# Performance work log

Hardware: AMD Instinct MI355X
Metric: run time of the kernel (lower is better)

The kernel has to match this reference:

```python
import jax, jax.numpy as jnp
import numpy as np

N_NODES = 50000
N_EDGES = 800000
D_IN = 128
N_HEADS = 8
D_OUT = 16  # per head; H*D = 128


def setup_inputs() -> dict:
    key = jax.random.key(0)
    ks = jax.random.split(key, 10)
    HD = N_HEADS * D_OUT
    nfeat = jax.random.normal(ks[0], (N_NODES, D_IN), dtype=jnp.float32)
    efeat = jax.random.normal(ks[1], (N_EDGES, D_IN), dtype=jnp.float32)
    src = jax.random.randint(ks[2], (N_EDGES,), 0, N_NODES, dtype=jnp.int32)
    dst = jax.random.randint(ks[3], (N_EDGES,), 0, N_NODES, dtype=jnp.int32)
    # parameters (Xavier-ish scale)
    W_fc = jax.random.normal(ks[4], (D_IN, HD), dtype=jnp.float32) * 0.05
    attn_l = jax.random.normal(ks[5], (N_HEADS, D_OUT), dtype=jnp.float32) * 0.05
    attn_r = jax.random.normal(ks[6], (N_HEADS, D_OUT), dtype=jnp.float32) * 0.05
    bias = jnp.zeros((HD,), dtype=jnp.float32)
    W_e = jax.random.normal(ks[7], (D_IN, HD), dtype=jnp.float32) * 0.05
    b_e = jnp.zeros((HD,), dtype=jnp.float32)
    return {"nfeat": nfeat, "efeat": efeat, "src": src, "dst": dst,
            "W_fc": W_fc, "attn_l": attn_l, "attn_r": attn_r, "bias": bias,
            "W_e": W_e, "b_e": b_e}


def reference(nfeat, efeat, src, dst, W_fc, attn_l, attn_r, bias, W_e, b_e):
    N = nfeat.shape[0]
    E = src.shape[0]
    H, D = attn_l.shape
    # ---- GATConv (DGL semantics, feat_drop=attn_drop=0, no residual/activation) ----
    hf = nfeat @ W_fc                      # [N, H*D]
    h = hf.reshape(N, H, D)                # [N, H, D]
    el = jnp.einsum('nhd,hd->nh', h, attn_l)   # [N, H]
    er = jnp.einsum('nhd,hd->nh', h, attn_r)   # [N, H]
    # per-edge scores: message src -> dst, softmax over incoming edges of dst
    e = jax.nn.leaky_relu(el[src] + er[dst], negative_slope=0.2)  # [E, H]
    m = jax.ops.segment_max(e, dst, num_segments=N)               # [N, H]
    m = jnp.where(jnp.isfinite(m), m, jnp.zeros_like(m))          # empty segments -> 0
    ex = jnp.exp(e - m[dst])                                      # [E, H]
    denom = jax.ops.segment_sum(ex, dst, num_segments=N)          # [N, H]
    a = ex / denom[dst]                                           # [E, H]
    agg = jax.ops.segment_sum(a[:, :, None] * h[src], dst, num_segments=N)  # [N, H, D]
    gat = agg.reshape(N, H * D) + bias                            # flatten(1) + bias
    # ---- skip term: fc(nfeat) / (in_degree + 1) ----
    ones = jnp.ones((E,), dtype=nfeat.dtype)
    indeg = jax.ops.segment_sum(ones, dst, num_segments=N)        # [N]
    sfeat = hf / (indeg + 1.0)[:, None]
    out = gat + sfeat
    # ---- econv: edge feature mean aggregation (copy_e + mean over in-edges) ----
    ef = efeat @ W_e + b_e                                        # [E, H*D]
    esum = jax.ops.segment_sum(ef, dst, num_segments=N)           # [N, H*D]
    h_e = esum / jnp.maximum(indeg, 1.0)[:, None]                 # zero-deg -> 0
    return out + h_e
```

## Files before the change

### kernel.cpp

```cpp
#include <hip/hip_runtime.h>
#include <math.h>

#define NN 50000
#define NE 800000
#define HD 128
#define NH 8
#define DO 16
#define NEG_BIG -3.0e38f

__device__ inline void fma4(float4& a, float s, const float4& b) {
    a.x = fmaf(s, b.x, a.x); a.y = fmaf(s, b.y, a.y);
    a.z = fmaf(s, b.z, a.z); a.w = fmaf(s, b.w, a.w);
}
__device__ inline void red4(float4& a, int off) {
    a.x += __shfl_xor(a.x, off); a.y += __shfl_xor(a.y, off);
    a.z += __shfl_xor(a.z, off); a.w += __shfl_xor(a.w, off);
}

__global__ void init_kernel(int* __restrict__ indeg) {
    int i = blockIdx.x * blockDim.x + threadIdx.x;
    if (i < NN) indeg[i] = 0;
}

__global__ void count_deg_kernel(const int* __restrict__ dst, int* __restrict__ indeg) {
    int e = blockIdx.x * blockDim.x + threadIdx.x;
    if (e < NE) atomicAdd(&indeg[dst[e]], 1);
}

__global__ __launch_bounds__(1024) void scan_kernel(const int* __restrict__ indeg,
                                                    int* __restrict__ offsets,
                                                    int* __restrict__ cursor) {
    __shared__ int part[1024];
    const int t = threadIdx.x;
    const int CH = (NN + 1023) / 1024;
    int b = t * CH, e = min(b + CH, NN);
    int s = 0;
    for (int i = b; i < e; ++i) s += indeg[i];
    part[t] = s;
    __syncthreads();
    for (int off = 1; off < 1024; off <<= 1) {
        int v = (t >= off) ? part[t - off] : 0;
        __syncthreads();
        part[t] += v;
        __syncthreads();
    }
    int base = (t == 0) ? 0 : part[t - 1];
    for (int i = b; i < e; ++i) {
        offsets[i] = base;
        cursor[i] = base;
        base += indeg[i];
    }
    if (t == 1023) offsets[NN] = base;
}

__global__ void scatter_kernel(const int* __restrict__ src, const int* __restrict__ dst,
                               int* __restrict__ cursor, int2* __restrict__ sorted) {
    int e = blockIdx.x * blockDim.x + threadIdx.x;
    if (e < NE) {
        int d = dst[e];
        int pos = atomicAdd(&cursor[d], 1);
        sorted[pos] = make_int2(src[e], e);
    }
}

template<bool FUSE_ATTN, bool ADD>
__global__ __launch_bounds__(256, 3) void gemm64_kernel(
    const float* __restrict__ A, const float* __restrict__ W,
    float* __restrict__ out,
    const float* __restrict__ attn_l, const float* __restrict__ attn_r,
    float* __restrict__ el, float* __restrict__ er)
{
    __shared__ float sA[64 * HD];
    __shared__ float sW[32 * HD];
    const int tid = threadIdx.x;
    const int tc = tid & 15;
    const int tr = tid >> 4;
    const int row0 = blockIdx.x * 64;

    const float4* Av = (const float4*)A;
    float4* sAv = (float4*)sA;
#pragma unroll
    for (int j = 0; j < 8; ++j) {
        int f = tid + j * 256;
        int r = f >> 5, g = f & 31;
        int gr = row0 + r;
        float4 v = make_float4(0.f, 0.f, 0.f, 0.f);
        if (gr < NN) v = Av[(size_t)gr * 32 + g];
        sAv[r * 32 + (g ^ ((r & 3) << 1))] = v;
    }

    float4 acc[4][2];
#pragma unroll
    for (int rj = 0; rj < 4; ++rj) {
        acc[rj][0] = make_float4(0.f, 0.f, 0.f, 0.f);
        acc[rj][1] = make_float4(0.f, 0.f, 0.f, 0.f);
    }

    const float4* Wv = (const float4*)W;
    float4* sWv = (float4*)sW;
    for (int kc = 0; kc < 4; ++kc) {
        __syncthreads();
#pragma unroll
        for (int j = 0; j < 4; ++j) {
            int f = tid + j * 256;
            sWv[f] = Wv[(size_t)(kc * 32 + (f >> 5)) * 32 + (f & 31)];
        }
        __syncthreads();
#pragma unroll 8
        for (int kk = 0; kk < 32; ++kk) {
            float4 w0 = sWv[kk * 32 + tc];
            float4 w1 = sWv[kk * 32 + 16 + tc];
            int k = kc * 32 + kk;
#pragma unroll
            for (int rj = 0; rj < 4; ++rj) {
                int r = tr + rj * 16;
                float a = sA[r * HD + (k ^ ((r & 3) << 3))];
                fma4(acc[rj][0], a, w0);
                fma4(acc[rj][1], a, w1);
            }
        }
    }

    if (FUSE_ATTN) {
        const int h1 = tc >> 2, q = tc & 3;
        float4 al0 = ((const float4*)attn_l)[h1 * 4 + q];
        float4 ar0 = ((const float4*)attn_r)[h1 * 4 + q];
        float4 al1 = ((const float4*)attn_l)[(h1 + 4) * 4 + q];
        float4 ar1 = ((const float4*)attn_r)[(h1 + 4) * 4 + q];
#pragma unroll
        for (int rj = 0; rj < 4; ++rj) {
            float sl0 = acc[rj][0].x * al0.x + acc[rj][0].y * al0.y + acc[rj][0].z * al0.z + acc[rj][0].w * al0.w;
            float sr0 = acc[rj][0].x * ar0.x + acc[rj][0].y * ar0.y + acc[rj][0].z * ar0.z + acc[rj][0].w * ar0.w;
            float sl1 = acc[rj][1].x * al1.x + acc[rj][1].y * al1.y + acc[rj][1].z * al1.z + acc[rj][1].w * al1.w;
            float sr1 = acc[rj][1].x * ar1.x + acc[rj][1].y * ar1.y + acc[rj][1].z * ar1.z + acc[rj][1].w * ar1.w;
            sl0 += __shfl_xor(sl0, 1); sl0 += __shfl_xor(sl0, 2);
            sr0 += __shfl_xor(sr0, 1); sr0 += __shfl_xor(sr0, 2);
            sl1 += __shfl_xor(sl1, 1); sl1 += __shfl_xor(sl1, 2);
            sr1 += __shfl_xor(sr1, 1); sr1 += __shfl_xor(sr1, 2);
            int gr = row0 + tr + rj * 16;
            if (q == 0 && gr < NN) {
                el[gr * NH + h1]     = sl0;  er[gr * NH + h1]     = sr0;
                el[gr * NH + h1 + 4] = sl1;  er[gr * NH + h1 + 4] = sr1;
            }
        }
    }

    float4* outv = (float4*)out;
#pragma unroll
    for (int rj = 0; rj < 4; ++rj) {
        int gr = row0 + tr + rj * 16;
        if (gr < NN) {
            size_t b = (size_t)gr * 32;
            if (ADD) {
                float4 p0 = outv[b + tc], p1 = outv[b + 16 + tc];
                p0.x += acc[rj][0].x; p0.y += acc[rj][0].y; p0.z += acc[rj][0].z; p0.w += acc[rj][0].w;
                p1.x += acc[rj][1].x; p1.y += acc[rj][1].y; p1.z += acc[rj][1].z; p1.w += acc[rj][1].w;
                outv[b + tc] = p0; outv[b + 16 + tc] = p1;
            } else {
                outv[b + tc] = acc[rj][0];
                outv[b + 16 + tc] = acc[rj][1];
            }
        }
    }
}

__global__ __launch_bounds__(256) void node_kernel(
    const int2* __restrict__ sorted, const int* __restrict__ offsets,
    const float* __restrict__ hf, const float* __restrict__ efeat,
    const float* __restrict__ el, const float* __restrict__ er,
    const float* __restrict__ bias, const float* __restrict__ b_e,
    float* __restrict__ out, float* __restrict__ eaggs)
{
    int wv   = threadIdx.x >> 6;
    int lane = threadIdx.x & 63;
    int node = blockIdx.x * 4 + wv;
    if (node >= NN) return;
    int beg = offsets[node];
    int end = offsets[node + 1];

    int h = lane & 7;
    float er_h = er[node * NH + h];
    float m = NEG_BIG, ssum = 0.0f;
    for (int i = beg + (lane >> 3); i < end; i += 8) {
        int s = sorted[i].x;
        float x = el[s * NH + h] + er_h;
        x = x > 0.0f ? x : 0.2f * x;
        if (x > m) { ssum = ssum * __expf(m - x) + 1.0f; m = x; }
        else        ssum += __expf(x - m);
    }
#pragma unroll
    for (int off = 8; off < 64; off <<= 1) {
        float mo = __shfl_xor(m, off);
        float so = __shfl_xor(ssum, off);
        float mn = fmaxf(m, mo);
        ssum = ssum * __expf(m - mn) + so * __expf(mo - mn);
        m = mn;
    }
    float r = ssum > 0.0f ? 1.0f / ssum : 0.0f;

    const int eslot = lane >> 4;
    const int cg    = lane & 15;
    const int h1 = cg >> 2, h2 = h1 + 4;
    float m1 = __shfl(m, h1), r1 = __shfl(r, h1);
    float m2 = __shfl(m, h2), r2 = __shfl(r, h2);
    float er1 = er[node * NH + h1];
    float er2 = er[node * NH + h2];

    const float4* hfv = (const float4*)hf;
    const float4* efv = (const float4*)efeat;
    float4 acc0 = make_float4(0.f,0.f,0.f,0.f), acc1 = acc0, ea0 = acc0, ea1 = acc0;

#pragma unroll 2
    for (int i0 = beg; i0 < end; i0 += 4) {
        int i = i0 + eslot;
        bool valid = i < end;
        int2 se = sorted[valid ? i : beg];
        int s = se.x;
        size_t eb = (size_t)se.y * 32;
        float x1 = el[s * NH + h1] + er1; x1 = x1 > 0.0f ? x1 : 0.2f * x1;
        float x2 = el[s * NH + h2] + er2; x2 = x2 > 0.0f ? x2 : 0.2f * x2;
        float vm = valid ? 1.0f : 0.0f;
        float w1 = __expf(x1 - m1) * r1 * vm;
        float w2 = __expf(x2 - m2) * r2 * vm;
        float4 hv0 = hfv[(size_t)s * 32 + cg];
        float4 hv1 = hfv[(size_t)s * 32 + 16 + cg];
        float4 ev0 = efv[eb + cg];
        float4 ev1 = efv[eb + 16 + cg];
        fma4(acc0, w1, hv0);
        fma4(acc1, w2, hv1);
        fma4(ea0, vm, ev0);
        fma4(ea1, vm, ev1);
    }

#pragma unroll
    for (int off = 16; off < 64; off <<= 1) {
        red4(acc0, off); red4(acc1, off);
        red4(ea0, off);  red4(ea1, off);
    }

    if (eslot == 0) {
        float deg   = (float)(end - beg);
        float rdeg  = 1.0f / fmaxf(deg, 1.0f);
        float rskip = 1.0f / (deg + 1.0f);
        float bsel  = deg > 0.0f ? 1.0f : 0.0f;
        size_t ob = (size_t)node * 32;
        float4 b0  = ((const float4*)bias)[cg],     b1  = ((const float4*)bias)[16 + cg];
        float4 be0 = ((const float4*)b_e)[cg],      be1 = ((const float4*)b_e)[16 + cg];
        float4 hf0 = hfv[ob + cg],                  hf1 = hfv[ob + 16 + cg];
        float4 o0, o1, g0, g1;
        o0.x = acc0.x + b0.x + hf0.x * rskip + bsel * be0.x;
        o0.y = acc0.y + b0.y + hf0.y * rskip + bsel * be0.y;
        o0.z = acc0.z + b0.z + hf0.z * rskip + bsel * be0.z;
        o0.w = acc0.w + b0.w + hf0.w * rskip + bsel * be0.w;
        o1.x = acc1.x + b1.x + hf1.x * rskip + bsel * be1.x;
        o1.y = acc1.y + b1.y + hf1.y * rskip + bsel * be1.y;
        o1.z = acc1.z + b1.z + hf1.z * rskip + bsel * be1.z;
        o1.w = acc1.w + b1.w + hf1.w * rskip + bsel * be1.w;
        g0.x = ea0.x * rdeg; g0.y = ea0.y * rdeg; g0.z = ea0.z * rdeg; g0.w = ea0.w * rdeg;
        g1.x = ea1.x * rdeg; g1.y = ea1.y * rdeg; g1.z = ea1.z * rdeg; g1.w = ea1.w * rdeg;
        ((float4*)out)[ob + cg]        = o0;
        ((float4*)out)[ob + 16 + cg]   = o1;
        ((float4*)eaggs)[ob + cg]      = g0;
        ((float4*)eaggs)[ob + 16 + cg] = g1;
    }
}

extern "C" void kernel_launch(void* const* d_in, const int* in_sizes, int n_in,
                              void* d_out, int out_size, void* d_ws, size_t ws_size,
                              hipStream_t stream) {
    const float* nfeat  = (const float*)d_in[0];
    const float* efeat  = (const float*)d_in[1];
    const int*   src    = (const int*)d_in[2];
    const int*   dst    = (const int*)d_in[3];
    const float* W_fc   = (const float*)d_in[4];
    const float* attn_l = (const float*)d_in[5];
    const float* attn_r = (const float*)d_in[6];
    const float* bias   = (const float*)d_in[7];
    const float* W_e    = (const float*)d_in[8];
    const float* b_e    = (const float*)d_in[9];
    float* out = (float*)d_out;

    float* ws = (float*)d_ws;
    size_t o = 0;
    float* hf      = ws + o; o += (size_t)NN * HD;
    float* el      = ws + o; o += (size_t)NN * NH;
    float* er      = ws + o; o += (size_t)NN * NH;
    int*   indeg   = (int*)(ws + o); o += NN;
    int*   offsets = (int*)(ws + o); o += NN + 1;
    int*   cursor  = (int*)(ws + o); o += NN;
    o = (o + 1) & ~(size_t)1;
    int2*  sorted  = (int2*)(ws + o); o += (size_t)NE * 2;
    float* eaggs   = ws + o; o += (size_t)NN * HD;

    init_kernel<<<(NN + 255) / 256, 256, 0, stream>>>(indeg);
    count_deg_kernel<<<(NE + 255) / 256, 256, 0, stream>>>(dst, indeg);
    scan_kernel<<<1, 1024, 0, stream>>>(indeg, offsets, cursor);
    scatter_kernel<<<(NE + 255) / 256, 256, 0, stream>>>(src, dst, cursor, sorted);

    gemm64_kernel<true, false><<<(NN + 63) / 64, 256, 0, stream>>>(
        nfeat, W_fc, hf, attn_l, attn_r, el, er);

    node_kernel<<<(NN + 3) / 4, 256, 0, stream>>>(sorted, offsets, hf, efeat,
                                                  el, er, bias, b_e, out, eaggs);

    gemm64_kernel<false, true><<<(NN + 63) / 64, 256, 0, stream>>>(
        eaggs, W_e, out, nullptr, nullptr, nullptr, nullptr);
}
```

Measured before the change: 881.1 us.

## Cache edge lists and scores in LDS; read GEMM weights directly from global

The node kernel now stages each node's first CAP sorted edges and their leaky-relu scores in shared memory during the softmax pass. The aggregation pass reuses them instead of re-reading sorted, el and er from global memory. The GEMM drops its shared-memory W staging and the extra barriers, reading W directly through the cache, and loads A as float4 from LDS. The trade-offs are more LDS per block in the node kernel (lowering occupancy) and more global/L2 traffic for W in the GEMM.

```diff
diff --git a/kernel.cpp b/kernel.cpp
--- a/kernel.cpp
+++ b/kernel.cpp
@@ -6,6 +6,7 @@
 #define HD 128
 #define NH 8
 #define DO 16
+#define CAP 96
 #define NEG_BIG -3.0e38f
 
 __device__ inline void fma4(float4& a, float s, const float4& b) {
@@ -64,21 +65,19 @@
 }
 
 template<bool FUSE_ATTN, bool ADD>
-__global__ __launch_bounds__(256, 3) void gemm64_kernel(
+__global__ __launch_bounds__(256) void gemm_kernel(
     const float* __restrict__ A, const float* __restrict__ W,
     float* __restrict__ out,
     const float* __restrict__ attn_l, const float* __restrict__ attn_r,
     float* __restrict__ el, float* __restrict__ er)
 {
-    __shared__ float sA[64 * HD];
-    __shared__ float sW[32 * HD];
+    __shared__ float4 sAv[64 * 32];
     const int tid = threadIdx.x;
     const int tc = tid & 15;
     const int tr = tid >> 4;
     const int row0 = blockIdx.x * 64;
 
     const float4* Av = (const float4*)A;
-    float4* sAv = (float4*)sA;
 #pragma unroll
     for (int j = 0; j < 8; ++j) {
         int f = tid + j * 256;
@@ -88,6 +87,7 @@
         if (gr < NN) v = Av[(size_t)gr * 32 + g];
         sAv[r * 32 + (g ^ ((r & 3) << 1))] = v;
     }
+    __syncthreads();
 
     float4 acc[4][2];
 #pragma unroll
@@ -97,24 +97,23 @@
     }
 
     const float4* Wv = (const float4*)W;
-    float4* sWv = (float4*)sW;
-    for (int kc = 0; kc < 4; ++kc) {
-        __syncthreads();
-#pragma unroll
-        for (int j = 0; j < 4; ++j) {
-            int f = tid + j * 256;
-            sWv[f] = Wv[(size_t)(kc * 32 + (f >> 5)) * 32 + (f & 31)];
-        }
-        __syncthreads();
-#pragma unroll 8
-        for (int kk = 0; kk < 32; ++kk) {
-            float4 w0 = sWv[kk * 32 + tc];
-            float4 w1 = sWv[kk * 32 + 16 + tc];
-            int k = kc * 32 + kk;
+#pragma unroll 2
+    for (int k0 = 0; k0 < 32; ++k0) {
+        float4 av[4];
+#pragma unroll
+        for (int rj = 0; rj < 4; ++rj) {
+            int r = tr + rj * 16;
+            av[rj] = sAv[r * 32 + (k0 ^ ((r & 3) << 1))];
+        }
+#pragma unroll
+        for (int kk = 0; kk < 4; ++kk) {
+            int k = k0 * 4 + kk;
+            float4 w0 = Wv[(size_t)k * 32 + tc];
+            float4 w1 = Wv[(size_t)k * 32 + 16 + tc];
 #pragma unroll
             for (int rj = 0; rj < 4; ++rj) {
-                int r = tr + rj * 16;
-                float a = sA[r * HD + (k ^ ((r & 3) << 3))];
+                float a = (kk == 0) ? av[rj].x : (kk == 1) ? av[rj].y
+                        : (kk == 2) ? av[rj].z : av[rj].w;
                 fma4(acc[rj][0], a, w0);
                 fma4(acc[rj][1], a, w1);
             }
@@ -171,20 +170,28 @@
     const float* __restrict__ bias, const float* __restrict__ b_e,
     float* __restrict__ out, float* __restrict__ eaggs)
 {
-    int wv   = threadIdx.x >> 6;
-    int lane = threadIdx.x & 63;
-    int node = blockIdx.x * 4 + wv;
-    if (node >= NN) return;
-    int beg = offsets[node];
-    int end = offsets[node + 1];
-
-    int h = lane & 7;
-    float er_h = er[node * NH + h];
+    __shared__ int2  eds[4][CAP];
+    __shared__ float xs[4][CAP * NH];
+    const int wv   = threadIdx.x >> 6;
+    const int lane = threadIdx.x & 63;
+    const int node = blockIdx.x * 4 + wv;
+    const bool act = node < NN;
+    const int beg = act ? offsets[node] : 0;
+    const int end = act ? offsets[node + 1] : 0;
+    const int deg = end - beg;
+
+    for (int i = lane; i < min(deg, CAP); i += 64)
+        eds[wv][i] = sorted[beg + i];
+    __syncthreads();
+
+    const int h = lane & 7, esub = lane >> 3;
+    float er_h = act ? er[node * NH + h] : 0.0f;
     float m = NEG_BIG, ssum = 0.0f;
-    for (int i = beg + (lane >> 3); i < end; i += 8) {
-        int s = sorted[i].x;
+    for (int i = esub; i < deg; i += 8) {
+        int s = (i < CAP) ? eds[wv][i].x : sorted[beg + i].x;
         float x = el[s * NH + h] + er_h;
         x = x > 0.0f ? x : 0.2f * x;
+        if (i < CAP) xs[wv][i * NH + h] = x;
         if (x > m) { ssum = ssum * __expf(m - x) + 1.0f; m = x; }
         else        ssum += __expf(x - m);
     }
@@ -197,33 +204,44 @@
         m = mn;
     }
     float r = ssum > 0.0f ? 1.0f / ssum : 0.0f;
+    __syncthreads();
 
     const int eslot = lane >> 4;
     const int cg    = lane & 15;
     const int h1 = cg >> 2, h2 = h1 + 4;
     float m1 = __shfl(m, h1), r1 = __shfl(r, h1);
     float m2 = __shfl(m, h2), r2 = __shfl(r, h2);
-    float er1 = er[node * NH + h1];
-    float er2 = er[node * NH + h2];
 
     const float4* hfv = (const float4*)hf;
     const float4* efv = (const float4*)efeat;
     float4 acc0 = make_float4(0.f,0.f,0.f,0.f), acc1 = acc0, ea0 = acc0, ea1 = acc0;
 
 #pragma unroll 2
-    for (int i0 = beg; i0 < end; i0 += 4) {
+    for (int i0 = 0; i0 < deg; i0 += 4) {
         int i = i0 + eslot;
-        bool valid = i < end;
-        int2 se = sorted[valid ? i : beg];
-        int s = se.x;
-        size_t eb = (size_t)se.y * 32;
-        float x1 = el[s * NH + h1] + er1; x1 = x1 > 0.0f ? x1 : 0.2f * x1;
-        float x2 = el[s * NH + h2] + er2; x2 = x2 > 0.0f ? x2 : 0.2f * x2;
+        bool valid = i < deg;
+        int s, eid;
+        float x1, x2;
+        if (i < CAP) {
+            int ii = valid ? i : 0;
+            int2 se = eds[wv][ii];
+            s = se.x; eid = se.y;
+            x1 = xs[wv][ii * NH + h1];
+            x2 = xs[wv][ii * NH + h2];
+        } else {
+            int2 se = sorted[beg + (valid ? i : 0)];
+            s = se.x; eid = se.y;
+            x1 = el[s * NH + h1] + er[node * NH + h1];
+            x2 = el[s * NH + h2] + er[node * NH + h2];
+            x1 = x1 > 0.0f ? x1 : 0.2f * x1;
+            x2 = x2 > 0.0f ? x2 : 0.2f * x2;
+        }
         float vm = valid ? 1.0f : 0.0f;
         float w1 = __expf(x1 - m1) * r1 * vm;
         float w2 = __expf(x2 - m2) * r2 * vm;
         float4 hv0 = hfv[(size_t)s * 32 + cg];
         float4 hv1 = hfv[(size_t)s * 32 + 16 + cg];
+        size_t eb = (size_t)eid * 32;
         float4 ev0 = efv[eb + cg];
         float4 ev1 = efv[eb + 16 + cg];
         fma4(acc0, w1, hv0);
@@ -238,15 +256,15 @@
         red4(ea0, off);  red4(ea1, off);
     }
 
-    if (eslot == 0) {
-        float deg   = (float)(end - beg);
-        float rdeg  = 1.0f / fmaxf(deg, 1.0f);
-        float rskip = 1.0f / (deg + 1.0f);
-        float bsel  = deg > 0.0f ? 1.0f : 0.0f;
+    if (act && eslot == 0) {
+        float degf  = (float)deg;
+        float rdeg  = 1.0f / fmaxf(degf, 1.0f);
+        float rskip = 1.0f / (degf + 1.0f);
+        float bsel  = deg > 0 ? 1.0f : 0.0f;
         size_t ob = (size_t)node * 32;
-        float4 b0  = ((const float4*)bias)[cg],     b1  = ((const float4*)bias)[16 + cg];
-        float4 be0 = ((const float4*)b_e)[cg],      be1 = ((const float4*)b_e)[16 + cg];
-        float4 hf0 = hfv[ob + cg],                  hf1 = hfv[ob + 16 + cg];
+        float4 b0  = ((const float4*)bias)[cg],  b1  = ((const float4*)bias)[16 + cg];
+        float4 be0 = ((const float4*)b_e)[cg],   be1 = ((const float4*)b_e)[16 + cg];
+        float4 hf0 = hfv[ob + cg],               hf1 = hfv[ob + 16 + cg];
         float4 o0, o1, g0, g1;
         o0.x = acc0.x + b0.x + hf0.x * rskip + bsel * be0.x;
         o0.y = acc0.y + b0.y + hf0.y * rskip + bsel * be0.y;
@@ -297,12 +315,12 @@
     scan_kernel<<<1, 1024, 0, stream>>>(indeg, offsets, cursor);
     scatter_kernel<<<(NE + 255) / 256, 256, 0, stream>>>(src, dst, cursor, sorted);
 
-    gemm64_kernel<true, false><<<(NN + 63) / 64, 256, 0, stream>>>(
+    gemm_kernel<true, false><<<(NN + 63) / 64, 256, 0, stream>>>(
         nfeat, W_fc, hf, attn_l, attn_r, el, er);
 
     node_kernel<<<(NN + 3) / 4, 256, 0, stream>>>(sorted, offsets, hf, efeat,
                                                   el, er, bias, b_e, out, eaggs);
 
-    gemm64_kernel<false, true><<<(NN + 63) / 64, 256, 0, stream>>>(
+    gemm_kernel<false, true><<<(NN + 63) / 64, 256, 0, stream>>>(
         eaggs, W_e, out, nullptr, nullptr, nullptr, nullptr);
 }
```

After: 884.4 us. About the same (+0.4%).
